# Optimization experiments

Hardware: AMD Instinct MI355X
Metric: run time of the kernel (lower is better)

## Reference

```python
import jax, jax.numpy as jnp
import numpy as np

B, C, T = 16, 8, 512
D_CHAR = D_SENT = D_CTX = 256
H_PW = H_PPH = H_IPH = 256
MLC = D_CHAR + D_SENT + D_CTX  # 768


def _gru_zero_h(x, Wih, bih, bhh, H):
    # PyTorch GRU step with h_prev = 0 (the module never passes h0, seq_len=1):
    #   r = sigmoid(Wir x + bir + bhr); z = sigmoid(Wiz x + biz + bhz)
    g = x @ Wih.T + bih  # [N, 3H]
    r = jax.nn.sigmoid(g[:, :H] + bhh[:H])
    z = jax.nn.sigmoid(g[:, H:2 * H] + bhh[H:2 * H])
    n = jnp.tanh(g[:, 2 * H:] + r * bhh[2 * H:])
    return (1.0 - z) * n


def setup_inputs() -> dict:
    key = jax.random.key(0)
    ks = jax.random.split(key, 16)
    s = 0.05
    inp = {
        "batch_character_representation": jax.random.normal(ks[0], (B, C, T, D_CHAR), jnp.float32),
        "batch_sentence_representation": jax.random.normal(ks[1], (B, C, D_SENT), jnp.float32),
        "batch_context_representation": jax.random.normal(ks[2], (B, C, D_CTX), jnp.float32),
        # GRU params (W_hh omitted: h_prev is always 0 so W_hh @ h == 0; b_hh kept)
        "pw_Wih": jax.random.normal(ks[3], (3 * H_PW, MLC + H_PW), jnp.float32) * s,
        "pw_bih": jax.random.normal(ks[4], (3 * H_PW,), jnp.float32) * s,
        "pw_bhh": jax.random.normal(ks[5], (3 * H_PW,), jnp.float32) * s,
        "pph_Wih": jax.random.normal(ks[6], (3 * H_PPH, MLC + H_PW + H_PPH), jnp.float32) * s,
        "pph_bih": jax.random.normal(ks[7], (3 * H_PPH,), jnp.float32) * s,
        "pph_bhh": jax.random.normal(ks[8], (3 * H_PPH,), jnp.float32) * s,
        "iph_Wih": jax.random.normal(ks[9], (3 * H_IPH, MLC + H_PW + H_PPH + H_IPH), jnp.float32) * s,
        "iph_bih": jax.random.normal(ks[10], (3 * H_IPH,), jnp.float32) * s,
        "iph_bhh": jax.random.normal(ks[11], (3 * H_IPH,), jnp.float32) * s,
        "pw_W": jax.random.normal(ks[12], (2, H_PW), jnp.float32) * s,
        "pw_b": jnp.zeros((2,), jnp.float32),
        "pph_W": jax.random.normal(ks[13], (2, H_PPH), jnp.float32) * s,
        "pph_b": jnp.zeros((2,), jnp.float32),
        "iph_W": jax.random.normal(ks[14], (2, H_IPH), jnp.float32) * s,
        "iph_b": jnp.zeros((2,), jnp.float32),
    }
    return inp


def reference(batch_character_representation, batch_sentence_representation,
              batch_context_representation, pw_Wih, pw_bih, pw_bhh,
              pph_Wih, pph_bih, pph_bhh, iph_Wih, iph_bih, iph_bhh,
              pw_W, pw_b, pph_W, pph_b, iph_W, iph_b):
    N = B * C
    chars = batch_character_representation.reshape(N, T, D_CHAR)
    sent = batch_sentence_representation.reshape(N, D_SENT)
    ctx = batch_context_representation.reshape(N, D_CTX)

    def step(carry, x_t):
        pw, pph, iph = carry  # [N,H] each
        base = jnp.concatenate([x_t, sent, ctx], axis=-1)  # [N, MLC]
        pw = _gru_zero_h(jnp.concatenate([base, pw], -1), pw_Wih, pw_bih, pw_bhh, H_PW)
        pph = _gru_zero_h(jnp.concatenate([base, pw, pph], -1), pph_Wih, pph_bih, pph_bhh, H_PPH)
        iph = _gru_zero_h(jnp.concatenate([base, pw, pph, iph], -1), iph_Wih, iph_bih, iph_bhh, H_IPH)
        return (pw, pph, iph), (pw, pph, iph)

    init = (jnp.zeros((N, H_PW), jnp.float32),
            jnp.zeros((N, H_PPH), jnp.float32),
            jnp.zeros((N, H_IPH), jnp.float32))
    _, (PWs, PPHs, IPHs) = jax.lax.scan(step, init, jnp.transpose(chars, (1, 0, 2)))

    def head(seq, W, b):  # seq: [T,N,H] -> [B,2,C,T]
        y = seq.transpose(1, 0, 2).reshape(B, C, T, -1) @ W.T + b
        return jnp.transpose(y, (0, 3, 1, 2))

    return (head(PWs, pw_W, pw_b), head(PPHs, pph_W, pph_b), head(IPHs, iph_W, iph_b))
```

## Files before the change

### kernel.cpp

```cpp
#include <hip/hip_runtime.h>
#include <hip/hip_bf16.h>
#include <stdint.h>

typedef __attribute__((ext_vector_type(8))) short bf16x8;
typedef __attribute__((ext_vector_type(4))) float f32x4;

#define N_SAMP 128
#define T_STEPS 512

#define WT_OFF    0u
#define GC_OFF    3538944u
#define RING_OFF  4718592u

__device__ __forceinline__ ushort f2bf(float f) {
    uint32_t u = __float_as_uint(f);
    uint32_t r = u + 0x7FFFu + ((u >> 16) & 1u);
    return (ushort)(r >> 16);
}
__device__ __forceinline__ float sigmoidf_(float x) { return 1.0f / (1.0f + __expf(-x)); }

__global__ void k_prep(const float* __restrict__ w0, const float* __restrict__ w1,
                       const float* __restrict__ w2, ushort* __restrict__ wt) {
    int idx = blockIdx.x * 256 + threadIdx.x;
    if (idx >= 1769472) return;
    int e, Ks, cols; const float* W;
    if (idx < 393216)      { e = idx;          Ks = 512;  cols = 1024; W = w0; }
    else if (idx < 983040) { e = idx - 393216; Ks = 768;  cols = 1280; W = w1; }
    else                   { e = idx - 983040; Ks = 1024; cols = 1536; W = w2; }
    int c = e / Ks, k = e % Ks;
    int b = c / 96, cc = c % 96, g = cc >> 5, d32 = cc & 31;
    int j = g * 256 + b * 32 + d32;
    int scol = (k < 256) ? k : (512 + k);
    wt[idx] = f2bf(W[(size_t)j * cols + scol]);
}

__global__ void k_gconst(const float* __restrict__ w0, const float* __restrict__ w1, const float* __restrict__ w2,
                         const float* __restrict__ bih0, const float* __restrict__ bih1, const float* __restrict__ bih2,
                         const float* __restrict__ bhh0, const float* __restrict__ bhh1, const float* __restrict__ bhh2,
                         const float* __restrict__ sent, const float* __restrict__ ctx,
                         float* __restrict__ gc) {
    int idx = blockIdx.x * 256 + threadIdx.x;
    if (idx >= 3 * 768 * 128) return;
    int n = idx & 127;
    int scc = idx >> 7;
    int c = scc % 768, s = scc / 768;
    const float* W   = (s == 0) ? w0 : ((s == 1) ? w1 : w2);
    const float* bih = (s == 0) ? bih0 : ((s == 1) ? bih1 : bih2);
    const float* bhh = (s == 0) ? bhh0 : ((s == 1) ? bhh1 : bhh2);
    int cols = 1024 + 256 * s;
    int b = c / 96, cc = c % 96, g = cc >> 5, d32 = cc & 31;
    int j = g * 256 + b * 32 + d32;
    float acc = bih[j] + ((g < 2) ? bhh[j] : 0.0f);
    const float4* wr4 = (const float4*)(W + (size_t)j * cols + 256);
    const float4* sn4 = (const float4*)(sent + (size_t)n * 256);
    const float4* cx4 = (const float4*)(ctx + (size_t)n * 256);
    #pragma unroll 4
    for (int k = 0; k < 64; k++) {
        float4 wv = wr4[k], sv = sn4[k];
        acc += wv.x * sv.x + wv.y * sv.y + wv.z * sv.z + wv.w * sv.w;
    }
    #pragma unroll 4
    for (int k = 0; k < 64; k++) {
        float4 wv = wr4[64 + k], cv = cx4[k];
        acc += wv.x * cv.x + wv.y * cv.y + wv.z * cv.z + wv.w * cv.w;
    }
    gc[(size_t)(s * 128 + n) * 768 + c] = acc;
}

__global__ void __launch_bounds__(128) k_step(
    const float* __restrict__ chars, const ushort* __restrict__ wt,
    const float* __restrict__ gc, ushort* __restrict__ ring,
    const float* __restrict__ bhh0, const float* __restrict__ bhh1, const float* __restrict__ bhh2,
    const float* __restrict__ hw0, const float* __restrict__ hw1, const float* __restrict__ hw2,
    const float* __restrict__ hb0, const float* __restrict__ hb1, const float* __restrict__ hb2,
    float* __restrict__ out, int stepi) {
    __shared__ ushort Alds[16384];
    __shared__ float  glds[16 * 96];

    int bx = blockIdx.x;
    int s  = bx >> 6;
    int r2 = bx & 63;
    int mt = r2 >> 3;
    int nb = r2 & 7;
    int t  = stepi - s;
    if (t < 0 || t >= T_STEPS) return;

    int Ks = 512 + 256 * s;
    const ushort* wts = wt + ((s == 0) ? 0 : ((s == 1) ? 393216 : 983040));
    int tid = threadIdx.x;

    #pragma unroll
    for (int i = 0; i < 4; i++) {
        int q  = tid + 128 * i;
        int r  = q >> 5;
        int ko = (q & 31) << 3;
        int n  = mt * 16 + r;
        const float* src = chars + ((size_t)n * T_STEPS + t) * 256 + ko;
        float4 f0 = *(const float4*)src;
        float4 f1 = *(const float4*)(src + 4);
        union { ushort u[8]; uint4 v; } pk;
        pk.u[0] = f2bf(f0.x); pk.u[1] = f2bf(f0.y); pk.u[2] = f2bf(f0.z); pk.u[3] = f2bf(f0.w);
        pk.u[4] = f2bf(f1.x); pk.u[5] = f2bf(f1.y); pk.u[6] = f2bf(f1.z); pk.u[7] = f2bf(f1.w);
        int pos = (ko >> 5) * 512 + (r + 16 * ((ko >> 3) & 3)) * 8;
        *(uint4*)(Alds + pos) = pk.v;
    }
    int nparts = s + 1;
    for (int p = 0; p < nparts; p++) {
        int slot = (p == s) ? ((t - 1) & 3) : (t & 3);
        const ushort* hsrc = ring + ((size_t)p * 4 + slot) * (128 * 256);
        #pragma unroll
        for (int i = 0; i < 4; i++) {
            int q  = tid + 128 * i;
            int r  = q >> 5;
            int ko = (q & 31) << 3;
            int n  = mt * 16 + r;
            uint4 v = *(const uint4*)(hsrc + (size_t)n * 256 + ko);
            int kg  = 256 + p * 256 + ko;
            int pos = (kg >> 5) * 512 + (r + 16 * ((kg >> 3) & 3)) * 8;
            *(uint4*)(Alds + pos) = v;
        }
    }
    __syncthreads();

    int w = tid >> 6, lane = tid & 63;
    int cb = nb * 96 + w * 48;
    f32x4 acc0 = {0.f, 0.f, 0.f, 0.f}, acc1 = {0.f, 0.f, 0.f, 0.f}, acc2 = {0.f, 0.f, 0.f, 0.f};
    const ushort* bp0 = wts + (size_t)(cb + (lane & 15)) * Ks + ((lane >> 4) << 3);
    const ushort* bp1 = bp0 + 16 * (size_t)Ks;
    const ushort* bp2 = bp0 + 32 * (size_t)Ks;
    const ushort* ap  = Alds + lane * 8;
    int nk = Ks >> 5;
    #pragma unroll 8
    for (int ks = 0; ks < nk; ks++) {
        bf16x8 a  = *(const bf16x8*)(ap + ks * 512);
        bf16x8 b0 = *(const bf16x8*)(bp0 + ks * 32);
        bf16x8 b1 = *(const bf16x8*)(bp1 + ks * 32);
        bf16x8 b2 = *(const bf16x8*)(bp2 + ks * 32);
        acc0 = __builtin_amdgcn_mfma_f32_16x16x32_bf16(a, b0, acc0, 0, 0, 0);
        acc1 = __builtin_amdgcn_mfma_f32_16x16x32_bf16(a, b1, acc1, 0, 0, 0);
        acc2 = __builtin_amdgcn_mfma_f32_16x16x32_bf16(a, b2, acc2, 0, 0, 0);
    }

    {
        int rbase = (lane >> 4) * 4;
        int c0 = w * 48 + (lane & 15);
        #pragma unroll
        for (int q = 0; q < 4; q++) {
            glds[(rbase + q) * 96 + c0]      = acc0[q];
            glds[(rbase + q) * 96 + c0 + 16] = acc1[q];
            glds[(rbase + q) * 96 + c0 + 32] = acc2[q];
        }
    }
    __syncthreads();

    {
        int sl = tid >> 3;
        int d0 = (tid & 7) * 4;
        int n  = mt * 16 + sl;
        const float* bhh = (s == 0) ? bhh0 : ((s == 1) ? bhh1 : bhh2);
        const float* hw  = (s == 0) ? hw0  : ((s == 1) ? hw1  : hw2);
        const float* hb  = (s == 0) ? hb0  : ((s == 1) ? hb1  : hb2);
        const float* gcp = gc + (size_t)(s * 128 + n) * 768 + nb * 96;
        float y0 = 0.f, y1 = 0.f;
        union { ushort u[4]; uint2 v; } hpk;
        #pragma unroll
        for (int dd = 0; dd < 4; dd++) {
            int d32 = d0 + dd;
            int d   = nb * 32 + d32;
            float rp = glds[sl * 96 + d32]      + gcp[d32];
            float zp = glds[sl * 96 + 32 + d32] + gcp[32 + d32];
            float np = glds[sl * 96 + 64 + d32] + gcp[64 + d32];
            float rg = sigmoidf_(rp);
            float zg = sigmoidf_(zp);
            float ng = tanhf(np + rg * bhh[512 + d]);
            float h  = (1.0f - zg) * ng;
            hpk.u[dd] = f2bf(h);
            y0 += h * hw[d];
            y1 += h * hw[256 + d];
        }
        *(uint2*)(ring + (((size_t)s * 4 + (t & 3)) * 128 + n) * 256 + nb * 32 + d0) = hpk.v;
        y0 += __shfl_xor(y0, 1); y0 += __shfl_xor(y0, 2); y0 += __shfl_xor(y0, 4);
        y1 += __shfl_xor(y1, 1); y1 += __shfl_xor(y1, 2); y1 += __shfl_xor(y1, 4);
        if ((tid & 7) == 0) {
            if (nb == 0) { y0 += hb[0]; y1 += hb[1]; }
            int bb = n >> 3, cc = n & 7;
            atomicAdd(out + (size_t)s * 131072 + (size_t)((bb * 2 + 0) * 8 + cc) * 512 + t, y0);
            atomicAdd(out + (size_t)s * 131072 + (size_t)((bb * 2 + 1) * 8 + cc) * 512 + t, y1);
        }
    }
}

extern "C" void kernel_launch(void* const* d_in, const int* in_sizes, int n_in,
                              void* d_out, int out_size, void* d_ws, size_t ws_size,
                              hipStream_t stream) {
    const float* chars = (const float*)d_in[0];
    const float* sent  = (const float*)d_in[1];
    const float* ctx   = (const float*)d_in[2];
    const float* w0    = (const float*)d_in[3];
    const float* bih0  = (const float*)d_in[4];
    const float* bhh0  = (const float*)d_in[5];
    const float* w1    = (const float*)d_in[6];
    const float* bih1  = (const float*)d_in[7];
    const float* bhh1  = (const float*)d_in[8];
    const float* w2    = (const float*)d_in[9];
    const float* bih2  = (const float*)d_in[10];
    const float* bhh2  = (const float*)d_in[11];
    const float* hw0   = (const float*)d_in[12];
    const float* hb0   = (const float*)d_in[13];
    const float* hw1   = (const float*)d_in[14];
    const float* hb1   = (const float*)d_in[15];
    const float* hw2   = (const float*)d_in[16];
    const float* hb2   = (const float*)d_in[17];

    char* ws = (char*)d_ws;
    ushort* wt   = (ushort*)(ws + WT_OFF);
    float*  gcb  = (float*)(ws + GC_OFF);
    ushort* ring = (ushort*)(ws + RING_OFF);
    float*  out  = (float*)d_out;

    hipMemsetAsync(d_out, 0, (size_t)out_size * sizeof(float), stream);
    hipMemsetAsync(ring, 0, (size_t)3 * 4 * 128 * 256 * 2, stream);

    k_prep<<<6912, 256, 0, stream>>>(w0, w1, w2, wt);
    k_gconst<<<1152, 256, 0, stream>>>(w0, w1, w2, bih0, bih1, bih2,
                                       bhh0, bhh1, bhh2, sent, ctx, gcb);
    for (int i = 0; i < T_STEPS + 2; i++) {
        k_step<<<192, 128, 0, stream>>>(chars, wt, gcb, ring,
                                        bhh0, bhh1, bhh2, hw0, hw1, hw2,
                                        hb0, hb1, hb2, out, i);
    }
}
```

Before: 5.597 ms.

## Replace per-step kernel launches with persistent kernel using global flag synchronization

```diff
diff --git a/kernel.cpp b/kernel.cpp
--- a/kernel.cpp
+++ b/kernel.cpp
@@ -4,12 +4,20 @@
 
 typedef __attribute__((ext_vector_type(8))) short bf16x8;
 typedef __attribute__((ext_vector_type(4))) float f32x4;
+typedef unsigned long long ull;
 
 #define N_SAMP 128
 #define T_STEPS 512
+#define RSLOTS 64
 
 #define WT_OFF    0u
 #define GC_OFF    3538944u
+#define FLAG_OFF  4718592u
+#define CONS_OFF  4767744u
+#define HIST_OFF  4816896u
+#define CB_OFF    17399808u
+#define NEED_MID  17399808ull
+#define NEED_FULL 50954240ull
 #define RING_OFF  4718592u
 
 __device__ __forceinline__ ushort f2bf(float f) {
@@ -18,6 +26,10 @@
     return (ushort)(r >> 16);
 }
 __device__ __forceinline__ float sigmoidf_(float x) { return 1.0f / (1.0f + __expf(-x)); }
+
+__device__ __forceinline__ void spin_ge(int* p, int v) {
+    while (__hip_atomic_load(p, __ATOMIC_RELAXED, __HIP_MEMORY_SCOPE_AGENT) < v) {}
+}
 
 __global__ void k_prep(const float* __restrict__ w0, const float* __restrict__ w1,
                        const float* __restrict__ w2, ushort* __restrict__ wt) {
@@ -67,6 +79,180 @@
     gc[(size_t)(s * 128 + n) * 768 + c] = acc;
 }
 
+__global__ void k_cprep(const float* __restrict__ chars, ushort* __restrict__ cb) {
+    int idx = blockIdx.x * 256 + threadIdx.x;
+    if (idx >= 2097152) return;
+    int q = idx & 511;
+    int gt = idx >> 9;
+    int t = gt & 511, g = gt >> 9;
+    int r = q >> 5, ko = (q & 31) << 3;
+    int n = g * 16 + r;
+    const float* src = chars + ((size_t)n * T_STEPS + t) * 256 + ko;
+    float4 f0 = *(const float4*)src;
+    float4 f1 = *(const float4*)(src + 4);
+    union { ushort u[8]; uint4 v; } pk;
+    pk.u[0] = f2bf(f0.x); pk.u[1] = f2bf(f0.y); pk.u[2] = f2bf(f0.z); pk.u[3] = f2bf(f0.w);
+    pk.u[4] = f2bf(f1.x); pk.u[5] = f2bf(f1.y); pk.u[6] = f2bf(f1.z); pk.u[7] = f2bf(f1.w);
+    int pos = (ko >> 5) * 512 + (r + 16 * ((ko >> 3) & 3)) * 8;
+    *(uint4*)(cb + (size_t)gt * 4096 + pos) = pk.v;
+}
+
+__global__ void __launch_bounds__(128) k_run(
+    const float* __restrict__ chars, const ushort* __restrict__ cb, int use_cb,
+    const ushort* __restrict__ wt, const float* __restrict__ gc,
+    ushort* __restrict__ hist, int* __restrict__ flag, int* __restrict__ cons,
+    const float* __restrict__ bhh0, const float* __restrict__ bhh1, const float* __restrict__ bhh2,
+    const float* __restrict__ hw0, const float* __restrict__ hw1, const float* __restrict__ hw2,
+    const float* __restrict__ hb0, const float* __restrict__ hb1, const float* __restrict__ hb2,
+    float* __restrict__ out) {
+    __shared__ ushort Alds[16384];
+    __shared__ float  glds[16 * 96];
+
+    int bx = blockIdx.x;
+    int s  = bx >> 6;
+    int r2 = bx & 63;
+    int g  = r2 >> 3;
+    int b  = r2 & 7;
+    int Ks = 512 + 256 * s;
+    const ushort* wts = wt + ((s == 0) ? 0 : ((s == 1) ? 393216 : 983040));
+    int tid = threadIdx.x;
+    int w = tid >> 6, lane = tid & 63;
+    const int CONS_FULL = (s == 0) ? 24 : ((s == 1) ? 16 : 8);
+    const float* bhh = (s == 0) ? bhh0 : ((s == 1) ? bhh1 : bhh2);
+    const float* hw  = (s == 0) ? hw0  : ((s == 1) ? hw1  : hw2);
+    const float* hb  = (s == 0) ? hb0  : ((s == 1) ? hb1  : hb2);
+
+    const ushort* bp0 = wts + (size_t)(b * 96 + w * 48 + (lane & 15)) * Ks + ((lane >> 4) << 3);
+    const ushort* bp1 = bp0 + 16 * (size_t)Ks;
+    const ushort* bp2 = bp0 + 32 * (size_t)Ks;
+    const ushort* ap  = Alds + lane * 8;
+    int nk = Ks >> 5;
+
+    for (int t = 0; t < T_STEPS; ++t) {
+        if (tid == 0) {
+            if (t > 0)   spin_ge(&flag[((s * 512) + (t - 1)) * 8 + g], 8);
+            if (s >= 1)  spin_ge(&flag[(((s - 1) * 512) + t) * 8 + g], 8);
+            if (s == 2)  spin_ge(&flag[t * 8 + g], 8);
+            if (t >= RSLOTS) spin_ge(&cons[((s * 512) + (t - RSLOTS)) * 8 + g], CONS_FULL);
+        }
+        __syncthreads();
+        asm volatile("" ::: "memory");
+
+        if (use_cb) {
+            const uint4* src = (const uint4*)(cb + ((size_t)(g * 512 + t)) * 4096);
+            uint4* dst = (uint4*)Alds;
+            #pragma unroll
+            for (int i = 0; i < 4; i++) dst[tid + 128 * i] = src[tid + 128 * i];
+        } else {
+            #pragma unroll
+            for (int i = 0; i < 4; i++) {
+                int q  = tid + 128 * i;
+                int r  = q >> 5;
+                int ko = (q & 31) << 3;
+                int n  = g * 16 + r;
+                const float* src = chars + ((size_t)n * T_STEPS + t) * 256 + ko;
+                float4 f0 = *(const float4*)src;
+                float4 f1 = *(const float4*)(src + 4);
+                union { ushort u[8]; uint4 v; } pk;
+                pk.u[0] = f2bf(f0.x); pk.u[1] = f2bf(f0.y); pk.u[2] = f2bf(f0.z); pk.u[3] = f2bf(f0.w);
+                pk.u[4] = f2bf(f1.x); pk.u[5] = f2bf(f1.y); pk.u[6] = f2bf(f1.z); pk.u[7] = f2bf(f1.w);
+                int pos = (ko >> 5) * 512 + (r + 16 * ((ko >> 3) & 3)) * 8;
+                *(uint4*)(Alds + pos) = pk.v;
+            }
+        }
+        for (int p = 0; p <= s; p++) {
+            int tp = (p == s) ? (t - 1) : t;
+            #pragma unroll
+            for (int i = 0; i < 4; i++) {
+                int q  = tid + 128 * i;
+                int r  = q >> 5;
+                int ko = (q & 31) << 3;
+                int n  = g * 16 + r;
+                int kg = 256 + p * 256 + ko;
+                int pos = (kg >> 5) * 512 + (r + 16 * ((ko >> 3) & 3)) * 8;
+                if (tp < 0) {
+                    *(ull*)(Alds + pos) = 0ull;
+                    *(ull*)(Alds + pos + 4) = 0ull;
+                } else {
+                    const ull* hp = (const ull*)(hist + (((size_t)p * RSLOTS + (tp & (RSLOTS - 1))) * 128 + n) * 256 + ko);
+                    ull lo = __hip_atomic_load(hp,     __ATOMIC_RELAXED, __HIP_MEMORY_SCOPE_AGENT);
+                    ull hi = __hip_atomic_load(hp + 1, __ATOMIC_RELAXED, __HIP_MEMORY_SCOPE_AGENT);
+                    *(ull*)(Alds + pos) = lo;
+                    *(ull*)(Alds + pos + 4) = hi;
+                }
+            }
+        }
+        __syncthreads();
+
+        if (tid == 0) {
+            if (t > 0)  __hip_atomic_fetch_add(&cons[((s * 512) + (t - 1)) * 8 + g], 1, __ATOMIC_RELAXED, __HIP_MEMORY_SCOPE_AGENT);
+            if (s >= 1) __hip_atomic_fetch_add(&cons[t * 8 + g], 1, __ATOMIC_RELAXED, __HIP_MEMORY_SCOPE_AGENT);
+            if (s == 2) __hip_atomic_fetch_add(&cons[(512 + t) * 8 + g], 1, __ATOMIC_RELAXED, __HIP_MEMORY_SCOPE_AGENT);
+        }
+
+        f32x4 acc0 = {0.f,0.f,0.f,0.f}, acc1 = {0.f,0.f,0.f,0.f}, acc2 = {0.f,0.f,0.f,0.f};
+        #pragma unroll 8
+        for (int ks = 0; ks < nk; ks++) {
+            bf16x8 a  = *(const bf16x8*)(ap + ks * 512);
+            bf16x8 b0 = *(const bf16x8*)(bp0 + ks * 32);
+            bf16x8 b1 = *(const bf16x8*)(bp1 + ks * 32);
+            bf16x8 b2 = *(const bf16x8*)(bp2 + ks * 32);
+            acc0 = __builtin_amdgcn_mfma_f32_16x16x32_bf16(a, b0, acc0, 0, 0, 0);
+            acc1 = __builtin_amdgcn_mfma_f32_16x16x32_bf16(a, b1, acc1, 0, 0, 0);
+            acc2 = __builtin_amdgcn_mfma_f32_16x16x32_bf16(a, b2, acc2, 0, 0, 0);
+        }
+        {
+            int rbase = (lane >> 4) * 4;
+            int c0 = w * 48 + (lane & 15);
+            #pragma unroll
+            for (int q = 0; q < 4; q++) {
+                glds[(rbase + q) * 96 + c0]      = acc0[q];
+                glds[(rbase + q) * 96 + c0 + 16] = acc1[q];
+                glds[(rbase + q) * 96 + c0 + 32] = acc2[q];
+            }
+        }
+        __syncthreads();
+
+        {
+            int sl = tid >> 3;
+            int d0 = (tid & 7) * 4;
+            int n  = g * 16 + sl;
+            const float* gcp = gc + (size_t)(s * 128 + n) * 768 + b * 96;
+            float y0 = 0.f, y1 = 0.f;
+            union { ushort u[4]; ull v; } hpk;
+            #pragma unroll
+            for (int dd = 0; dd < 4; dd++) {
+                int d32 = d0 + dd;
+                int d   = b * 32 + d32;
+                float rp = glds[sl * 96 + d32]      + gcp[d32];
+                float zp = glds[sl * 96 + 32 + d32] + gcp[32 + d32];
+                float np = glds[sl * 96 + 64 + d32] + gcp[64 + d32];
+                float rg = sigmoidf_(rp);
+                float zg = sigmoidf_(zp);
+                float ng = tanhf(np + rg * bhh[512 + d]);
+                float h  = (1.0f - zg) * ng;
+                hpk.u[dd] = f2bf(h);
+                y0 += h * hw[d];
+                y1 += h * hw[256 + d];
+            }
+            ull* hp = (ull*)(hist + (((size_t)s * RSLOTS + (t & (RSLOTS - 1))) * 128 + n) * 256 + b * 32 + d0);
+            __hip_atomic_store(hp, hpk.v, __ATOMIC_RELAXED, __HIP_MEMORY_SCOPE_AGENT);
+            y0 += __shfl_xor(y0, 1); y0 += __shfl_xor(y0, 2); y0 += __shfl_xor(y0, 4);
+            y1 += __shfl_xor(y1, 1); y1 += __shfl_xor(y1, 2); y1 += __shfl_xor(y1, 4);
+            if ((tid & 7) == 0) {
+                if (b == 0) { y0 += hb[0]; y1 += hb[1]; }
+                int bb = n >> 3, cc = n & 7;
+                atomicAdd(out + (size_t)s * 131072 + (size_t)((bb * 2 + 0) * 8 + cc) * 512 + t, y0);
+                atomicAdd(out + (size_t)s * 131072 + (size_t)((bb * 2 + 1) * 8 + cc) * 512 + t, y1);
+            }
+        }
+        __syncthreads();
+        if (tid == 0) {
+            __hip_atomic_fetch_add(&flag[((s * 512) + t) * 8 + g], 1, __ATOMIC_RELEASE, __HIP_MEMORY_SCOPE_AGENT);
+        }
+    }
+}
+
 __global__ void __launch_bounds__(128) k_step(
     const float* __restrict__ chars, const ushort* __restrict__ wt,
     const float* __restrict__ gc, ushort* __restrict__ ring,
@@ -123,9 +309,9 @@
     __syncthreads();
 
     int w = tid >> 6, lane = tid & 63;
-    int cb = nb * 96 + w * 48;
-    f32x4 acc0 = {0.f, 0.f, 0.f, 0.f}, acc1 = {0.f, 0.f, 0.f, 0.f}, acc2 = {0.f, 0.f, 0.f, 0.f};
-    const ushort* bp0 = wts + (size_t)(cb + (lane & 15)) * Ks + ((lane >> 4) << 3);
+    int cbcol = nb * 96 + w * 48;
+    f32x4 acc0 = {0.f,0.f,0.f,0.f}, acc1 = {0.f,0.f,0.f,0.f}, acc2 = {0.f,0.f,0.f,0.f};
+    const ushort* bp0 = wts + (size_t)(cbcol + (lane & 15)) * Ks + ((lane >> 4) << 3);
     const ushort* bp1 = bp0 + 16 * (size_t)Ks;
     const ushort* bp2 = bp0 + 32 * (size_t)Ks;
     const ushort* ap  = Alds + lane * 8;
@@ -140,7 +326,6 @@
         acc1 = __builtin_amdgcn_mfma_f32_16x16x32_bf16(a, b1, acc1, 0, 0, 0);
         acc2 = __builtin_amdgcn_mfma_f32_16x16x32_bf16(a, b2, acc2, 0, 0, 0);
     }
-
     {
         int rbase = (lane >> 4) * 4;
         int c0 = w * 48 + (lane & 15);
@@ -215,18 +400,32 @@
     char* ws = (char*)d_ws;
     ushort* wt   = (ushort*)(ws + WT_OFF);
     float*  gcb  = (float*)(ws + GC_OFF);
-    ushort* ring = (ushort*)(ws + RING_OFF);
     float*  out  = (float*)d_out;
 
     hipMemsetAsync(d_out, 0, (size_t)out_size * sizeof(float), stream);
-    hipMemsetAsync(ring, 0, (size_t)3 * 4 * 128 * 256 * 2, stream);
-
     k_prep<<<6912, 256, 0, stream>>>(w0, w1, w2, wt);
     k_gconst<<<1152, 256, 0, stream>>>(w0, w1, w2, bih0, bih1, bih2,
                                        bhh0, bhh1, bhh2, sent, ctx, gcb);
-    for (int i = 0; i < T_STEPS + 2; i++) {
-        k_step<<<192, 128, 0, stream>>>(chars, wt, gcb, ring,
-                                        bhh0, bhh1, bhh2, hw0, hw1, hw2,
-                                        hb0, hb1, hb2, out, i);
-    }
-}
+
+    if (ws_size >= NEED_MID) {
+        int*    flag = (int*)(ws + FLAG_OFF);
+        int*    cons = (int*)(ws + CONS_OFF);
+        ushort* hist = (ushort*)(ws + HIST_OFF);
+        ushort* cbuf = (ushort*)(ws + CB_OFF);
+        int use_cb = (ws_size >= NEED_FULL) ? 1 : 0;
+        hipMemsetAsync(ws + FLAG_OFF, 0, 98304, stream);
+        if (use_cb) k_cprep<<<8192, 256, 0, stream>>>(chars, cbuf);
+        k_run<<<192, 128, 0, stream>>>(chars, use_cb ? cbuf : (const ushort*)nullptr, use_cb,
+                                       wt, gcb, hist, flag, cons,
+                                       bhh0, bhh1, bhh2, hw0, hw1, hw2,
+                                       hb0, hb1, hb2, out);
+    } else {
+        ushort* ring = (ushort*)(ws + RING_OFF);
+        hipMemsetAsync(ring, 0, (size_t)3 * 4 * 128 * 256 * 2, stream);
+        for (int i = 0; i < T_STEPS + 2; i++) {
+            k_step<<<192, 128, 0, stream>>>(chars, wt, gcb, ring,
+                                            bhh0, bhh1, bhh2, hw0, hw1, hw2,
+                                            hb0, hb1, hb2, out, i);
+        }
+    }
+}
```

New measurement: 9.151 ms. 1.63x slower.

## Replace per-step kernel launches with a persistent kernel using flag-based cross-block sync

Applied to the files above, without the earlier changes.

```diff
diff --git a/kernel.cpp b/kernel.cpp
--- a/kernel.cpp
+++ b/kernel.cpp
@@ -4,12 +4,18 @@
 
 typedef __attribute__((ext_vector_type(8))) short bf16x8;
 typedef __attribute__((ext_vector_type(4))) float f32x4;
-
-#define N_SAMP 128
+typedef unsigned long long ull;
+
 #define T_STEPS 512
+#define RS3 32
+#define GL 100
 
 #define WT_OFF    0u
 #define GC_OFF    3538944u
+#define PROG_OFF  4718592u
+#define HIST3_OFF 4722688u
+#define CB_OFF    13111296u
+#define NEED_NEW  46665728ull
 #define RING_OFF  4718592u
 
 __device__ __forceinline__ ushort f2bf(float f) {
@@ -18,6 +24,293 @@
     return (ushort)(r >> 16);
 }
 __device__ __forceinline__ float sigmoidf_(float x) { return 1.0f / (1.0f + __expf(-x)); }
+
+__device__ __forceinline__ void gld16(bf16x8& d, const void* p) {
+    asm volatile("global_load_dwordx4 %0, %1, off" : "=&v"(d) : "v"(p) : "memory");
+}
+__device__ __forceinline__ void gld16c(bf16x8& d, const void* p) {
+    asm volatile("global_load_dwordx4 %0, %1, off sc0 sc1" : "=&v"(d) : "v"(p) : "memory");
+}
+__device__ __forceinline__ void gld16u(uint4& d, const void* p) {
+    asm volatile("global_load_dwordx4 %0, %1, off" : "=&v"(d) : "v"(p) : "memory");
+}
+__device__ __forceinline__ void llc_store8(void* p, ull v) {
+    asm volatile("global_store_dwordx2 %0, %1, off sc0 sc1" :: "v"(p), "v"(v) : "memory");
+}
+#define VWAIT(N) { asm volatile("s_waitcnt vmcnt(" #N ")" ::: "memory"); __builtin_amdgcn_sched_barrier(0); }
+__device__ __forceinline__ void drain_vmem() {
+    asm volatile("s_waitcnt vmcnt(0)" ::: "memory");
+}
+
+__global__ void k_prep2(const float* __restrict__ w0, const float* __restrict__ w1,
+                        const float* __restrict__ w2, ushort* __restrict__ wt2) {
+    int idx = blockIdx.x * 256 + threadIdx.x;
+    if (idx >= 1769472) return;
+    int e, Ks, cols, s; const float* W;
+    if (idx < 393216)      { e = idx;          Ks = 512;  cols = 1024; W = w0; s = 0; }
+    else if (idx < 983040) { e = idx - 393216; Ks = 768;  cols = 1280; W = w1; s = 1; }
+    else                   { e = idx - 983040; Ks = 1024; cols = 1536; W = w2; s = 2; }
+    int c = e / Ks, k = e % Ks;
+    int j = c / 96, cc = c % 96;
+    int g = cc >> 5, d32 = cc & 31;
+    int ct = cc >> 4, cl = cc & 15;
+    int srcrow = g * 256 + j * 32 + d32;
+    int scol = (k < 256) ? k : (512 + k);
+    int kc = k >> 8, kl = k & 255, ks = kl >> 5, ko = kl & 31;
+    int lane = ((ko >> 3) << 4) | cl, elem = ko & 7;
+    size_t sbase = (s == 0) ? 0u : ((s == 1) ? 393216u : 983040u);
+    size_t dst = sbase + (size_t)j * (s + 2) * 24576 +
+                 ((size_t)(kc * 6 + ct) * 8 + ks) * 512 + lane * 8 + elem;
+    wt2[dst] = f2bf(W[(size_t)srcrow * cols + scol]);
+}
+
+__global__ void k_gconst2(const float* __restrict__ w0, const float* __restrict__ w1, const float* __restrict__ w2,
+                          const float* __restrict__ bih0, const float* __restrict__ bih1, const float* __restrict__ bih2,
+                          const float* __restrict__ bhh0, const float* __restrict__ bhh1, const float* __restrict__ bhh2,
+                          const float* __restrict__ sent, const float* __restrict__ ctx,
+                          float* __restrict__ gcf) {
+    int idx = blockIdx.x * 256 + threadIdx.x;
+    if (idx >= 294912) return;
+    int q = idx & 3; int r1 = idx >> 2;
+    int lane = r1 & 63; int r2 = r1 >> 6;
+    int rt = r2 & 7; int r3 = r2 >> 3;
+    int ct = r3 % 6; int sj = r3 / 6;
+    int s = sj >> 3, j = sj & 7;
+    const float* W   = (s == 0) ? w0 : ((s == 1) ? w1 : w2);
+    const float* bih = (s == 0) ? bih0 : ((s == 1) ? bih1 : bih2);
+    const float* bhh = (s == 0) ? bhh0 : ((s == 1) ? bhh1 : bhh2);
+    int cols = 1024 + 256 * s;
+    int cc = ct * 16 + (lane & 15);
+    int g = cc >> 5, d32 = cc & 31;
+    int jr = g * 256 + j * 32 + d32;
+    int n = rt * 16 + ((lane >> 4) << 2) + q;
+    float acc = bih[jr] + ((g < 2) ? bhh[jr] : 0.0f);
+    const float4* wr4 = (const float4*)(W + (size_t)jr * cols + 256);
+    const float4* sn4 = (const float4*)(sent + (size_t)n * 256);
+    const float4* cx4 = (const float4*)(ctx + (size_t)n * 256);
+    #pragma unroll 4
+    for (int k = 0; k < 64; k++) {
+        float4 wv = wr4[k], sv = sn4[k];
+        acc += wv.x * sv.x + wv.y * sv.y + wv.z * sv.z + wv.w * sv.w;
+    }
+    #pragma unroll 4
+    for (int k = 0; k < 64; k++) {
+        float4 wv = wr4[64 + k], cv = cx4[k];
+        acc += wv.x * cv.x + wv.y * cv.y + wv.z * cv.z + wv.w * cv.w;
+    }
+    gcf[idx] = acc;
+}
+
+__global__ void k_cprep(const float* __restrict__ chars, ushort* __restrict__ cb) {
+    int idx = blockIdx.x * 256 + threadIdx.x;
+    if (idx >= 2097152) return;
+    int q = idx & 511;
+    int gt = idx >> 9;
+    int t = gt & 511, g = gt >> 9;
+    int r = q >> 5, ko = (q & 31) << 3;
+    int n = g * 16 + r;
+    const float* src = chars + ((size_t)n * T_STEPS + t) * 256 + ko;
+    float4 f0 = *(const float4*)src;
+    float4 f1 = *(const float4*)(src + 4);
+    union { ushort u[8]; uint4 v; } pk;
+    pk.u[0] = f2bf(f0.x); pk.u[1] = f2bf(f0.y); pk.u[2] = f2bf(f0.z); pk.u[3] = f2bf(f0.w);
+    pk.u[4] = f2bf(f1.x); pk.u[5] = f2bf(f1.y); pk.u[6] = f2bf(f1.z); pk.u[7] = f2bf(f1.w);
+    int pos = (ko >> 5) * 512 + (r + 16 * ((ko >> 3) & 3)) * 8;
+    *(uint4*)(cb + (size_t)gt * 4096 + pos) = pk.v;
+}
+
+__global__ void __launch_bounds__(512) k_run3(
+    const ushort* __restrict__ cb, const ushort* __restrict__ wt2,
+    const float* __restrict__ gcf, ushort* __restrict__ hist, int* __restrict__ prog,
+    const float* __restrict__ bhh0, const float* __restrict__ bhh1, const float* __restrict__ bhh2,
+    const float* __restrict__ hw0, const float* __restrict__ hw1, const float* __restrict__ hw2,
+    const float* __restrict__ hb0, const float* __restrict__ hb1, const float* __restrict__ hb2,
+    float* __restrict__ out) {
+    __shared__ ushort Blds[73728];
+    __shared__ ushort hlds[4096];
+
+    int bid = blockIdx.x;
+    int s = bid >> 3, j = bid & 7;
+    int tid = threadIdx.x;
+    int w = tid >> 6, lane = tid & 63, la = lane & 15;
+    const float* bhh = (s == 0) ? bhh0 : ((s == 1) ? bhh1 : bhh2);
+    const float* hw  = (s == 0) ? hw0  : ((s == 1) ? hw1  : hw2);
+    const float* hb  = (s == 0) ? hb0  : ((s == 1) ? hb1  : hb2);
+    const ushort* wt2s = wt2 + ((s == 0) ? 0u : ((s == 1) ? 393216u : 983040u))
+                       + (size_t)j * (s + 2) * 24576;
+
+#define FILLB(SRC, DST) { const uint4* sp_ = (const uint4*)(wt2s + (size_t)(SRC) * 24576); \
+    uint4* dp_ = (uint4*)(Blds + (DST) * 24576); \
+    _Pragma("unroll") for (int i_ = 0; i_ < 6; i_++) dp_[tid + 512 * i_] = sp_[tid + 512 * i_]; }
+
+    if (s == 0)      { FILLB(0, 0) FILLB(1, 1) }
+    else if (s == 1) { FILLB(0, 0) FILLB(1, 1) FILLB(2, 2) }
+    else             { FILLB(0, 0) FILLB(3, 1) }
+    __syncthreads();
+
+    float4 G[6];
+    #pragma unroll
+    for (int ct = 0; ct < 6; ct++)
+        G[ct] = ((const float4*)gcf)[(((size_t)(s * 8 + j) * 6 + ct) * 8 + w) * 64 + lane];
+    float bhna = bhh[512 + j * 32 + la];
+    float bhnb = bhh[512 + j * 32 + 16 + la];
+    float hwa0 = hw[j * 32 + la], hwb0 = hw[j * 32 + 16 + la];
+    float hwa1 = hw[256 + j * 32 + la], hwb1 = hw[256 + j * 32 + 16 + la];
+    float hbi0 = (j == 0) ? hb[0] : 0.f, hbi1 = (j == 0) ? hb[1] : 0.f;
+    int* pself = prog + (s * 8 + j) * 16;
+
+#define MCH(REG, AR) { _Pragma("unroll") for (int ks_ = 0; ks_ < 8; ks_++) { \
+    const ushort* bb_ = Blds + (REG) * 24576 + ks_ * 512 + lane * 8; \
+    bf16x8 a_ = AR[ks_]; \
+    acc[0] = __builtin_amdgcn_mfma_f32_16x16x32_bf16(a_, *(const bf16x8*)(bb_        ), acc[0], 0, 0, 0); \
+    acc[1] = __builtin_amdgcn_mfma_f32_16x16x32_bf16(a_, *(const bf16x8*)(bb_ +  4096), acc[1], 0, 0, 0); \
+    acc[2] = __builtin_amdgcn_mfma_f32_16x16x32_bf16(a_, *(const bf16x8*)(bb_ +  8192), acc[2], 0, 0, 0); \
+    acc[3] = __builtin_amdgcn_mfma_f32_16x16x32_bf16(a_, *(const bf16x8*)(bb_ + 12288), acc[3], 0, 0, 0); \
+    acc[4] = __builtin_amdgcn_mfma_f32_16x16x32_bf16(a_, *(const bf16x8*)(bb_ + 16384), acc[4], 0, 0, 0); \
+    acc[5] = __builtin_amdgcn_mfma_f32_16x16x32_bf16(a_, *(const bf16x8*)(bb_ + 20480), acc[5], 0, 0, 0); } }
+
+#define ISSUE_CB(AR) { const ushort* cs_ = cb + (((size_t)w * 512 + t) << 12); \
+    _Pragma("unroll") for (int ks_ = 0; ks_ < 8; ks_++) gld16(AR[ks_], cs_ + ks_ * 512 + lane * 8); }
+#define ISSUE_H(AR, P, SLOT) { const ushort* hs_ = hist + ((((size_t)(P) * RS3 + (SLOT)) * 8 + w) << 12); \
+    _Pragma("unroll") for (int ks_ = 0; ks_ < 8; ks_++) gld16c(AR[ks_], hs_ + ks_ * 512 + lane * 8); }
+
+    for (int t = 0; t < T_STEPS; ++t) {
+        if (tid < 24) {
+            int grp = tid >> 3, i8 = tid & 7;
+            int want = 0; bool act = false;
+            if (s == 0)      { if (grp == 0) { want = t; act = (t > 0); }
+                               else          { want = t - RS3 + 1; act = (t >= RS3); } }
+            else if (s == 1) { if (grp == 0) { want = t + 1; act = true; }
+                               else if (grp == 1) { want = t; act = (t > 0); }
+                               else { want = t - RS3 + 1; act = (t >= RS3); } }
+            else             { if (grp <= 1) { want = t + 1; act = true; }
+                               else { want = t; act = (t > 0); } }
+            if (act) {
+                int* p = prog + (grp * 8 + i8) * 16;
+                while (__hip_atomic_load(p, __ATOMIC_RELAXED, __HIP_MEMORY_SCOPE_AGENT) < want) {}
+            }
+        }
+        __syncthreads();
+
+        f32x4 acc[6];
+        #pragma unroll
+        for (int ct = 0; ct < 6; ct++) acc[ct] = (f32x4){0.f, 0.f, 0.f, 0.f};
+
+        bf16x8 A0[8], A1[8], A2[8];
+        int slot_t  = t & (RS3 - 1);
+        int slot_t1 = (t - 1) & (RS3 - 1);
+
+        if (s == 0) {
+            ISSUE_CB(A0)
+            if (t > 0) { ISSUE_H(A1, 0, slot_t1) VWAIT(8) } else { VWAIT(0) }
+            MCH(0, A0)
+            if (t > 0) { VWAIT(0) MCH(1, A1) }
+        } else if (s == 1) {
+            ISSUE_CB(A0)
+            ISSUE_H(A1, 0, slot_t)
+            if (t > 0) { ISSUE_H(A2, 1, slot_t1) VWAIT(16) } else { VWAIT(8) }
+            MCH(0, A0)
+            VWAIT(0)
+            MCH(1, A1)
+            if (t > 0) MCH(2, A2)
+        } else {
+            uint4 Br[6];
+            { const uint4* sp = (const uint4*)(wt2s + (size_t)1 * 24576);
+              #pragma unroll
+              for (int i = 0; i < 6; i++) gld16u(Br[i], sp + tid + 512 * i); }
+            ISSUE_CB(A0)
+            ISSUE_H(A1, 0, slot_t)
+            VWAIT(8)
+            { uint4* dp = (uint4*)(Blds + 2 * 24576);
+              #pragma unroll
+              for (int i = 0; i < 6; i++) dp[tid + 512 * i] = Br[i]; }
+            MCH(0, A0)
+            VWAIT(0)
+            __syncthreads();
+            MCH(2, A1)
+            { const uint4* sp = (const uint4*)(wt2s + (size_t)2 * 24576);
+              #pragma unroll
+              for (int i = 0; i < 6; i++) gld16u(Br[i], sp + tid + 512 * i); }
+            ISSUE_H(A0, 1, slot_t)
+            if (t > 0) ISSUE_H(A1, 2, slot_t1)
+            VWAIT(0)
+            __syncthreads();
+            { uint4* dp = (uint4*)(Blds + 2 * 24576);
+              #pragma unroll
+              for (int i = 0; i < 6; i++) dp[tid + 512 * i] = Br[i]; }
+            __syncthreads();
+            MCH(2, A0)
+            if (t > 0) MCH(1, A1)
+        }
+
+        float ha[4], hbv[4];
+        #pragma unroll
+        for (int q = 0; q < 4; q++) {
+            float r1 = sigmoidf_(acc[0][q] + G[0][q]);
+            float z1 = sigmoidf_(acc[2][q] + G[2][q]);
+            float n1 = tanhf(acc[4][q] + G[4][q] + r1 * bhna);
+            ha[q] = (1.0f - z1) * n1;
+            float r2 = sigmoidf_(acc[1][q] + G[1][q]);
+            float z2 = sigmoidf_(acc[3][q] + G[3][q]);
+            float n2 = tanhf(acc[5][q] + G[5][q] + r2 * bhnb);
+            hbv[q] = (1.0f - z2) * n2;
+        }
+        #pragma unroll
+        for (int q = 0; q < 4; q++) {
+            int smp = w * 16 + ((lane >> 4) << 2) + q;
+            hlds[smp * 32 + la]      = f2bf(ha[q]);
+            hlds[smp * 32 + 16 + la] = f2bf(hbv[q]);
+        }
+        __syncthreads();
+
+        {
+            int rt = tid >> 6, rem = tid & 63, r = rem >> 2, oc = rem & 3;
+            const ushort* hsp = hlds + (rt * 16 + r) * 32 + oc * 8;
+            ull lo = *(const ull*)(hsp);
+            ull hi = *(const ull*)(hsp + 4);
+            ushort* dst = hist + (((size_t)s * RS3 + slot_t) * 8 + rt) * 4096
+                        + j * 512 + (r + 16 * oc) * 8;
+            llc_store8(dst, lo);
+            llc_store8(dst + 4, hi);
+        }
+        drain_vmem();
+        __syncthreads();
+        if (tid == 0) {
+            __hip_atomic_fetch_add(pself, 1, __ATOMIC_RELAXED, __HIP_MEMORY_SCOPE_AGENT);
+        }
+
+        {
+            float y0[4], y1[4];
+            #pragma unroll
+            for (int q = 0; q < 4; q++) {
+                y0[q] = ha[q] * hwa0 + hbv[q] * hwb0;
+                y1[q] = ha[q] * hwa1 + hbv[q] * hwb1;
+            }
+            #pragma unroll
+            for (int m = 1; m <= 8; m <<= 1) {
+                #pragma unroll
+                for (int q = 0; q < 4; q++) {
+                    y0[q] += __shfl_xor(y0[q], m);
+                    y1[q] += __shfl_xor(y1[q], m);
+                }
+            }
+            if (la == 0) {
+                #pragma unroll
+                for (int q = 0; q < 4; q++) {
+                    int n = w * 16 + ((lane >> 4) << 2) + q;
+                    int bi = n >> 3, ci = n & 7;
+                    atomicAdd(out + ((size_t)s << 17) + (size_t)((bi * 2 + 0) * 8 + ci) * 512 + t, y0[q] + hbi0);
+                    atomicAdd(out + ((size_t)s << 17) + (size_t)((bi * 2 + 1) * 8 + ci) * 512 + t, y1[q] + hbi1);
+                }
+            }
+        }
+        drain_vmem();
+    }
+#undef MCH
+#undef ISSUE_CB
+#undef ISSUE_H
+#undef FILLB
+}
 
 __global__ void k_prep(const float* __restrict__ w0, const float* __restrict__ w1,
                        const float* __restrict__ w2, ushort* __restrict__ wt) {
@@ -29,9 +322,9 @@
     else                   { e = idx - 983040; Ks = 1024; cols = 1536; W = w2; }
     int c = e / Ks, k = e % Ks;
     int b = c / 96, cc = c % 96, g = cc >> 5, d32 = cc & 31;
-    int j = g * 256 + b * 32 + d32;
+    int jr = g * 256 + b * 32 + d32;
     int scol = (k < 256) ? k : (512 + k);
-    wt[idx] = f2bf(W[(size_t)j * cols + scol]);
+    wt[idx] = f2bf(W[(size_t)jr * cols + scol]);
 }
 
 __global__ void k_gconst(const float* __restrict__ w0, const float* __restrict__ w1, const float* __restrict__ w2,
@@ -49,9 +342,9 @@
     const float* bhh = (s == 0) ? bhh0 : ((s == 1) ? bhh1 : bhh2);
     int cols = 1024 + 256 * s;
     int b = c / 96, cc = c % 96, g = cc >> 5, d32 = cc & 31;
-    int j = g * 256 + b * 32 + d32;
-    float acc = bih[j] + ((g < 2) ? bhh[j] : 0.0f);
-    const float4* wr4 = (const float4*)(W + (size_t)j * cols + 256);
+    int jr = g * 256 + b * 32 + d32;
+    float acc = bih[jr] + ((g < 2) ? bhh[jr] : 0.0f);
+    const float4* wr4 = (const float4*)(W + (size_t)jr * cols + 256);
     const float4* sn4 = (const float4*)(sent + (size_t)n * 256);
     const float4* cx4 = (const float4*)(ctx + (size_t)n * 256);
     #pragma unroll 4
@@ -75,7 +368,7 @@
     const float* __restrict__ hb0, const float* __restrict__ hb1, const float* __restrict__ hb2,
     float* __restrict__ out, int stepi) {
     __shared__ ushort Alds[16384];
-    __shared__ float  glds[16 * 96];
+    __shared__ float  glds[16 * GL];
 
     int bx = blockIdx.x;
     int s  = bx >> 6;
@@ -123,9 +416,9 @@
     __syncthreads();
 
     int w = tid >> 6, lane = tid & 63;
-    int cb = nb * 96 + w * 48;
-    f32x4 acc0 = {0.f, 0.f, 0.f, 0.f}, acc1 = {0.f, 0.f, 0.f, 0.f}, acc2 = {0.f, 0.f, 0.f, 0.f};
-    const ushort* bp0 = wts + (size_t)(cb + (lane & 15)) * Ks + ((lane >> 4) << 3);
+    int cbcol = nb * 96 + w * 48;
+    f32x4 acc0 = {0,0,0,0}, acc1 = {0,0,0,0}, acc2 = {0,0,0,0};
+    const ushort* bp0 = wts + (size_t)(cbcol + (lane & 15)) * Ks + ((lane >> 4) << 3);
     const ushort* bp1 = bp0 + 16 * (size_t)Ks;
     const ushort* bp2 = bp0 + 32 * (size_t)Ks;
     const ushort* ap  = Alds + lane * 8;
@@ -140,15 +433,14 @@
         acc1 = __builtin_amdgcn_mfma_f32_16x16x32_bf16(a, b1, acc1, 0, 0, 0);
         acc2 = __builtin_amdgcn_mfma_f32_16x16x32_bf16(a, b2, acc2, 0, 0, 0);
     }
-
     {
         int rbase = (lane >> 4) * 4;
         int c0 = w * 48 + (lane & 15);
         #pragma unroll
         for (int q = 0; q < 4; q++) {
-            glds[(rbase + q) * 96 + c0]      = acc0[q];
-            glds[(rbase + q) * 96 + c0 + 16] = acc1[q];
-            glds[(rbase + q) * 96 + c0 + 32] = acc2[q];
+            glds[(rbase + q) * GL + c0]      = acc0[q];
+            glds[(rbase + q) * GL + c0 + 16] = acc1[q];
+            glds[(rbase + q) * GL + c0 + 32] = acc2[q];
         }
     }
     __syncthreads();
@@ -167,9 +459,9 @@
         for (int dd = 0; dd < 4; dd++) {
             int d32 = d0 + dd;
             int d   = nb * 32 + d32;
-            float rp = glds[sl * 96 + d32]      + gcp[d32];
-            float zp = glds[sl * 96 + 32 + d32] + gcp[32 + d32];
-            float np = glds[sl * 96 + 64 + d32] + gcp[64 + d32];
+            float rp = glds[sl * GL + d32]      + gcp[d32];
+            float zp = glds[sl * GL + 32 + d32] + gcp[32 + d32];
+            float np = glds[sl * GL + 64 + d32] + gcp[64 + d32];
             float rg = sigmoidf_(rp);
             float zg = sigmoidf_(zp);
             float ng = tanhf(np + rg * bhh[512 + d]);
@@ -183,9 +475,9 @@
         y1 += __shfl_xor(y1, 1); y1 += __shfl_xor(y1, 2); y1 += __shfl_xor(y1, 4);
         if ((tid & 7) == 0) {
             if (nb == 0) { y0 += hb[0]; y1 += hb[1]; }
-            int bb = n >> 3, cc = n & 7;
-            atomicAdd(out + (size_t)s * 131072 + (size_t)((bb * 2 + 0) * 8 + cc) * 512 + t, y0);
-            atomicAdd(out + (size_t)s * 131072 + (size_t)((bb * 2 + 1) * 8 + cc) * 512 + t, y1);
+            int bi = n >> 3, ci = n & 7;
+            atomicAdd(out + (size_t)s * 131072 + (size_t)((bi * 2 + 0) * 8 + ci) * 512 + t, y0);
+            atomicAdd(out + (size_t)s * 131072 + (size_t)((bi * 2 + 1) * 8 + ci) * 512 + t, y1);
         }
     }
 }
@@ -213,20 +505,36 @@
     const float* hb2   = (const float*)d_in[17];
 
     char* ws = (char*)d_ws;
-    ushort* wt   = (ushort*)(ws + WT_OFF);
-    float*  gcb  = (float*)(ws + GC_OFF);
-    ushort* ring = (ushort*)(ws + RING_OFF);
-    float*  out  = (float*)d_out;
+    float* out = (float*)d_out;
 
     hipMemsetAsync(d_out, 0, (size_t)out_size * sizeof(float), stream);
-    hipMemsetAsync(ring, 0, (size_t)3 * 4 * 128 * 256 * 2, stream);
-
-    k_prep<<<6912, 256, 0, stream>>>(w0, w1, w2, wt);
-    k_gconst<<<1152, 256, 0, stream>>>(w0, w1, w2, bih0, bih1, bih2,
-                                       bhh0, bhh1, bhh2, sent, ctx, gcb);
-    for (int i = 0; i < T_STEPS + 2; i++) {
-        k_step<<<192, 128, 0, stream>>>(chars, wt, gcb, ring,
-                                        bhh0, bhh1, bhh2, hw0, hw1, hw2,
-                                        hb0, hb1, hb2, out, i);
-    }
-}
+
+    if (ws_size >= NEED_NEW) {
+        ushort* wt2  = (ushort*)(ws + WT_OFF);
+        float*  gcf  = (float*)(ws + GC_OFF);
+        int*    prg  = (int*)(ws + PROG_OFF);
+        ushort* hist = (ushort*)(ws + HIST3_OFF);
+        ushort* cbuf = (ushort*)(ws + CB_OFF);
+        hipMemsetAsync(ws + PROG_OFF, 0, 4096, stream);
+        k_prep2<<<6912, 256, 0, stream>>>(w0, w1, w2, wt2);
+        k_gconst2<<<1152, 256, 0, stream>>>(w0, w1, w2, bih0, bih1, bih2,
+                                            bhh0, bhh1, bhh2, sent, ctx, gcf);
+        k_cprep<<<8192, 256, 0, stream>>>(chars, cbuf);
+        k_run3<<<24, 512, 0, stream>>>(cbuf, wt2, gcf, hist, prg,
+                                       bhh0, bhh1, bhh2, hw0, hw1, hw2,
+                                       hb0, hb1, hb2, out);
+    } else {
+        ushort* wt  = (ushort*)(ws + WT_OFF);
+        float*  gcb = (float*)(ws + GC_OFF);
+        ushort* ring = (ushort*)(ws + RING_OFF);
+        k_prep<<<6912, 256, 0, stream>>>(w0, w1, w2, wt);
+        k_gconst<<<1152, 256, 0, stream>>>(w0, w1, w2, bih0, bih1, bih2,
+                                           bhh0, bhh1, bhh2, sent, ctx, gcb);
+        hipMemsetAsync(ring, 0, (size_t)3 * 4 * 128 * 256 * 2, stream);
+        for (int i = 0; i < T_STEPS + 2; i++) {
+            k_step<<<192, 128, 0, stream>>>(chars, wt, gcb, ring,
+                                            bhh0, bhh1, bhh2, hw0, hw1, hw2,
+                                            hb0, hb1, hb2, out, i);
+        }
+    }
+}
```

Measured after the change: 7.113 ms. +27.1%, slower.
